# Performance work log

Measured on AMD Instinct MI355X. Metric: run time of the kernel, lower is better.

The kernel has to match this reference:

```python
import jax, jax.numpy as jnp
import numpy as np

N_NODES = 65536
N_EDGES = 786432
N_RELS = 8
IN_DIM = 128
HID = 128
N_CLASSES = 10
N_GRAPHS = 64


def setup_inputs() -> dict:
    key = jax.random.key(0)
    ks = jax.random.split(key, 10)
    h = jax.random.normal(ks[0], (N_NODES, IN_DIM), dtype=jnp.float32)
    s = 1.0 / np.sqrt(IN_DIM)
    W1 = jax.random.normal(ks[1], (N_RELS, IN_DIM, HID), dtype=jnp.float32) * s
    W1_self = jax.random.normal(ks[2], (IN_DIM, HID), dtype=jnp.float32) * s
    b1 = jnp.zeros((HID,), dtype=jnp.float32)
    sh = 1.0 / np.sqrt(HID)
    W2 = jax.random.normal(ks[3], (N_RELS, HID, HID), dtype=jnp.float32) * sh
    W2_self = jax.random.normal(ks[4], (HID, HID), dtype=jnp.float32) * sh
    b2 = jnp.zeros((HID,), dtype=jnp.float32)
    Wc = jax.random.normal(ks[5], (HID, N_CLASSES), dtype=jnp.float32) * sh
    bc = jnp.zeros((N_CLASSES,), dtype=jnp.float32)
    src = jax.random.randint(ks[6], (N_EDGES,), 0, N_NODES, dtype=jnp.int32)
    dst = jax.random.randint(ks[7], (N_EDGES,), 0, N_NODES, dtype=jnp.int32)
    etype = jax.random.randint(ks[8], (N_EDGES,), 0, N_RELS, dtype=jnp.int32)
    # 64 batched graphs of 1024 nodes each (contiguous node blocks)
    graph_ids = (jnp.arange(N_NODES, dtype=jnp.int32) // (N_NODES // N_GRAPHS)).astype(jnp.int32)
    return dict(h=h, W1=W1, W1_self=W1_self, b1=b1, W2=W2, W2_self=W2_self,
                b2=b2, Wc=Wc, bc=bc, src=src, dst=dst, etype=etype,
                graph_ids=graph_ids)


def _relgraphconv(h, W, W_self, b, src, dst, etype):
    # DGL RelGraphConv (regularizer=None, self_loop=True, bias=True, no norm):
    # out[v] = sum_{e: dst(e)=v} W[etype(e)] @ h[src(e)]  +  W_self @ h[v] + b
    # Transform all nodes under each relation (R is small), then gather per-edge.
    xw = jnp.einsum('ni,rio->rno', h, W)          # [R, N, HID]
    msg = xw[etype, src]                           # [E, HID] gather
    agg = jax.ops.segment_sum(msg, dst, num_segments=N_NODES)  # scatter-add
    return agg + h @ W_self + b


def reference(h, W1, W1_self, b1, W2, W2_self, b2, Wc, bc,
              src, dst, etype, graph_ids):
    h1 = jax.nn.relu(_relgraphconv(h, W1, W1_self, b1, src, dst, etype))
    h2 = jax.nn.relu(_relgraphconv(h1, W2, W2_self, b2, src, dst, etype))
    pooled = jax.ops.segment_max(h2, graph_ids, num_segments=N_GRAPHS)  # [G, HID]
    return pooled @ Wc + bc
```

## Files before the change

kernel.cpp:

```cpp
#include <hip/hip_runtime.h>
#include <hip/hip_bf16.h>


#define N_NODES 65536
#define N_EDGES 786432
#define DIM 128
#define NT 9
#define XW_LD (NT * DIM)
#define N_GRAPHS 64

typedef unsigned int uint;
typedef unsigned short ushort;
typedef __attribute__((ext_vector_type(8))) short short8;
typedef __attribute__((ext_vector_type(4))) float f32x4;

__device__ inline ushort f2b(float f) {
  uint u = __float_as_uint(f);
  u += 0x7fff + ((u >> 16) & 1);
  return (ushort)(u >> 16);
}
__device__ inline float b2f(ushort h) { return __uint_as_float(((uint)h) << 16); }
__device__ inline float blo(uint v) { return __uint_as_float(v << 16); }
__device__ inline float bhi(uint v) { return __uint_as_float(v & 0xffff0000u); }

__device__ inline void gl_lds16(const void* g, void* l) {
  __builtin_amdgcn_global_load_lds(
      (const __attribute__((address_space(1))) unsigned int*)g,
      (__attribute__((address_space(3))) unsigned int*)l, 16, 0, 0);
}

__global__ __launch_bounds__(256) void f32_to_bf16_vec(const float* __restrict__ x,
                                                       ushort* __restrict__ y, int n4) {
  int i = blockIdx.x * 256 + threadIdx.x;
  if (i >= n4) return;
  float4 v = ((const float4*)x)[i];
  ushort4 o;
  o.x = f2b(v.x); o.y = f2b(v.y); o.z = f2b(v.z); o.w = f2b(v.w);
  ((ushort4*)y)[i] = o;
}

__global__ __launch_bounds__(256) void wconv_all(const float* __restrict__ W1,
                                                 const float* __restrict__ W1s,
                                                 const float* __restrict__ W2,
                                                 const float* __restrict__ W2s,
                                                 ushort* __restrict__ Wt1,
                                                 ushort* __restrict__ Wt2) {
  int b = blockIdx.x;
  const float* S;
  ushort* D;
  int tile;
  if (b < 9) { D = Wt1; tile = b; S = (b < 8) ? (W1 + (size_t)b * 16384) : W1s; }
  else       { D = Wt2; tile = b - 9; S = (tile < 8) ? (W2 + (size_t)tile * 16384) : W2s; }
  for (int i = threadIdx.x; i < 16384; i += 256) {
    int n = i >> 7, k = i & 127;
    D[((size_t)tile * 128 + n) * 128 + k] = f2b(S[k * 128 + n]);
  }
}

__global__ __launch_bounds__(256) void fill_bins_sliced(const int* __restrict__ src,
                                                        const int* __restrict__ dst,
                                                        const int* __restrict__ et,
                                                        int* __restrict__ cnt,
                                                        uint* __restrict__ bins) {
  int slice = blockIdx.x & 7;
  int e = (blockIdx.x >> 3) * 256 + threadIdx.x;
  if (e >= N_EDGES) return;
  int d = dst[e];
  if ((d >> 13) != slice) return;
  int r = atomicAdd(&cnt[d], 1);
  if (r < 64) bins[((size_t)d << 6) + r] = (uint)src[e] * 576u + (uint)et[e] * 64u;
}

__global__ __launch_bounds__(256, 4) void gemm_bk64(const ushort* __restrict__ A,
                                                    const ushort* __restrict__ Bt,
                                                    ushort* __restrict__ C, int ldc) {
  __shared__ char lds[32768];
  const int bid = blockIdx.x;
  const int swz = (bid & 7) * 576 + (bid >> 3);
  const int bm = swz / 9, bn = swz % 9;
  const char* Ag = (const char*)(A + (size_t)bm * 128 * 128);
  const char* Bg = (const char*)(Bt + (size_t)bn * 128 * 128);
  const int tid = threadIdx.x, wv = tid >> 6, ln = tid & 63;
  const int wm = wv >> 1, wn = wv & 1, lr = ln & 15, kq = ln >> 4;

  f32x4 acc[4][4];
#pragma unroll
  for (int m = 0; m < 4; ++m)
#pragma unroll
    for (int n = 0; n < 4; ++n) acc[m][n] = (f32x4){0.f, 0.f, 0.f, 0.f};

#pragma unroll
  for (int kt = 0; kt < 2; ++kt) {
    if (kt) __syncthreads();
#pragma unroll
    for (int it = 0; it < 4; ++it) {
      int chunk = it * 4096 + wv * 1024;
      int p = chunk + ln * 16;
      int row = p >> 7, inb = p & 127;
      int sw = inb ^ ((row & 7) << 4);
      size_t gb = (size_t)row * 256 + (size_t)kt * 128 + sw;
      gl_lds16(Ag + gb, lds + chunk);
      gl_lds16(Bg + gb, lds + 16384 + chunk);
    }
    asm volatile("s_waitcnt vmcnt(0)" ::: "memory");
    __syncthreads();
#pragma unroll
    for (int k2 = 0; k2 < 2; ++k2) {
      const int kb = k2 * 64 + kq * 16;
      short8 a[4], b[4];
#pragma unroll
      for (int m = 0; m < 4; ++m) {
        int row = wm * 64 + m * 16 + lr;
        a[m] = *(const short8*)(lds + ((row * 128 + kb) ^ ((row & 7) << 4)));
      }
#pragma unroll
      for (int n = 0; n < 4; ++n) {
        int col = wn * 64 + n * 16 + lr;
        b[n] = *(const short8*)(lds + 16384 + ((col * 128 + kb) ^ ((col & 7) << 4)));
      }
#pragma unroll
      for (int m = 0; m < 4; ++m)
#pragma unroll
        for (int n = 0; n < 4; ++n)
          acc[m][n] = __builtin_amdgcn_mfma_f32_16x16x32_bf16(a[m], b[n], acc[m][n], 0, 0, 0);
    }
  }

  __syncthreads();
#pragma unroll
  for (int m = 0; m < 4; ++m) {
    int rb0 = wm * 64 + m * 16 + kq * 4;
#pragma unroll
    for (int n = 0; n < 4; ++n) {
      int col = wn * 64 + n * 16 + lr;
#pragma unroll
      for (int e = 0; e < 4; ++e) {
        int row = rb0 + e;
        int off = (row * 256 + col * 2) ^ ((row & 7) << 4);
        *(ushort*)(lds + off) = f2b(acc[m][n][e]);
      }
    }
  }
  __syncthreads();
  char* Cg = (char*)C + (size_t)(bm * 128) * (size_t)ldc * 2 + (size_t)bn * 256;
#pragma unroll
  for (int it = 0; it < 8; ++it) {
    int p = it * 4096 + tid * 16;
    int row = p >> 8, inb = p & 255;
    short8 v = *(const short8*)(lds + row * 256 + (inb ^ ((row & 7) << 4)));
    *(short8*)(Cg + (size_t)row * (size_t)ldc * 2 + inb) = v;
  }
}

template <bool POOL>
__global__ __launch_bounds__(256) void gather_out(const uint* __restrict__ XWu,
                                                  const uint* __restrict__ bins,
                                                  const int* __restrict__ cnt,
                                                  const float* __restrict__ bias,
                                                  uint* __restrict__ hout,
                                                  ushort* __restrict__ partial2) {
  __shared__ ushort pm[4][128];
  int node = (blockIdx.x * 256 + threadIdx.x) >> 6;
  int w = threadIdx.x >> 6;
  int ln = threadIdx.x & 63;
  int ne = __builtin_amdgcn_readfirstlane(cnt[node]);
  if (ne > 64) ne = 64;
  uint sv = XWu[(size_t)node * 576 + 512 + ln];
  float2 bv = ((const float2*)bias)[ln];
  uint mv = bins[((size_t)node << 6) + ln];
  float2 acc = {0.f, 0.f};

  int i = 0;
  for (; i + 8 <= ne; i += 8) {
    uint v0 = XWu[(uint)__builtin_amdgcn_readlane((int)mv, i + 0) + ln];
    uint v1 = XWu[(uint)__builtin_amdgcn_readlane((int)mv, i + 1) + ln];
    uint v2 = XWu[(uint)__builtin_amdgcn_readlane((int)mv, i + 2) + ln];
    uint v3 = XWu[(uint)__builtin_amdgcn_readlane((int)mv, i + 3) + ln];
    uint v4 = XWu[(uint)__builtin_amdgcn_readlane((int)mv, i + 4) + ln];
    uint v5 = XWu[(uint)__builtin_amdgcn_readlane((int)mv, i + 5) + ln];
    uint v6 = XWu[(uint)__builtin_amdgcn_readlane((int)mv, i + 6) + ln];
    uint v7 = XWu[(uint)__builtin_amdgcn_readlane((int)mv, i + 7) + ln];
    acc.x += blo(v0); acc.y += bhi(v0);
    acc.x += blo(v1); acc.y += bhi(v1);
    acc.x += blo(v2); acc.y += bhi(v2);
    acc.x += blo(v3); acc.y += bhi(v3);
    acc.x += blo(v4); acc.y += bhi(v4);
    acc.x += blo(v5); acc.y += bhi(v5);
    acc.x += blo(v6); acc.y += bhi(v6);
    acc.x += blo(v7); acc.y += bhi(v7);
  }
  for (; i + 4 <= ne; i += 4) {
    uint v0 = XWu[(uint)__builtin_amdgcn_readlane((int)mv, i + 0) + ln];
    uint v1 = XWu[(uint)__builtin_amdgcn_readlane((int)mv, i + 1) + ln];
    uint v2 = XWu[(uint)__builtin_amdgcn_readlane((int)mv, i + 2) + ln];
    uint v3 = XWu[(uint)__builtin_amdgcn_readlane((int)mv, i + 3) + ln];
    acc.x += blo(v0); acc.y += bhi(v0);
    acc.x += blo(v1); acc.y += bhi(v1);
    acc.x += blo(v2); acc.y += bhi(v2);
    acc.x += blo(v3); acc.y += bhi(v3);
  }
  for (; i < ne; ++i) {
    uint v = XWu[(uint)__builtin_amdgcn_readlane((int)mv, i) + ln];
    acc.x += blo(v); acc.y += bhi(v);
  }

  float r0 = fmaxf(acc.x + blo(sv) + bv.x, 0.f);
  float r1 = fmaxf(acc.y + bhi(sv) + bv.y, 0.f);
  if (POOL) {
    pm[w][ln * 2] = f2b(r0);
    pm[w][ln * 2 + 1] = f2b(r1);
    __syncthreads();
    int t = threadIdx.x;
    if (t < 128) {
      float m = fmaxf(fmaxf(b2f(pm[0][t]), b2f(pm[1][t])),
                      fmaxf(b2f(pm[2][t]), b2f(pm[3][t])));
      partial2[(size_t)blockIdx.x * 128 + t] = f2b(m);
    }
  } else {
    hout[(size_t)node * 64 + ln] = (uint)f2b(r0) | ((uint)f2b(r1) << 16);
  }
}

__global__ __launch_bounds__(256) void classify2(const ushort* __restrict__ partial2,
                                                 const float* __restrict__ Wc,
                                                 const float* __restrict__ bc,
                                                 float* __restrict__ out) {
  __shared__ float red[2][128];
  __shared__ float pooled[128];
  int g = blockIdx.x, t = threadIdx.x;
  int d = t & 127, half = t >> 7;
  const ushort* base = partial2 + ((size_t)g * 256 + half * 128) * 128;
  float m = 0.f;
  for (int i = 0; i < 128; ++i) m = fmaxf(m, b2f(base[i * 128 + d]));
  red[half][d] = m;
  __syncthreads();
  if (t < 128) pooled[t] = fmaxf(red[0][t], red[1][t]);
  __syncthreads();
  if (t < 10) {
    float s = bc[t];
    for (int dd = 0; dd < DIM; ++dd) s += pooled[dd] * Wc[dd * 10 + t];
    out[g * 10 + t] = s;
  }
}

extern "C" void kernel_launch(void* const* d_in, const int* in_sizes, int n_in,
                              void* d_out, int out_size, void* d_ws, size_t ws_size,
                              hipStream_t stream) {
  const float* h       = (const float*)d_in[0];
  const float* W1      = (const float*)d_in[1];
  const float* W1_self = (const float*)d_in[2];
  const float* b1      = (const float*)d_in[3];
  const float* W2      = (const float*)d_in[4];
  const float* W2_self = (const float*)d_in[5];
  const float* b2      = (const float*)d_in[6];
  const float* Wc      = (const float*)d_in[7];
  const float* bc      = (const float*)d_in[8];
  const int* src   = (const int*)d_in[9];
  const int* dst   = (const int*)d_in[10];
  const int* etype = (const int*)d_in[11];
  float* out = (float*)d_out;

  char* ws = (char*)d_ws;
  ushort* XW      = (ushort*)(ws);
  ushort* hb      = (ushort*)(ws + 150994944);
  ushort* h1b     = (ushort*)(ws + 167772160);
  ushort* Wt1c    = (ushort*)(ws + 184549376);
  ushort* Wt2c    = (ushort*)(ws + 184844288);
  int*    cnt     = (int*)(ws + 185139200);
  uint*   bins    = (uint*)(ws + 185401344);
  ushort* partial2= (ushort*)(ws + 202178560);

  const int n4_h = N_NODES * DIM / 4;
  const int g_h = n4_h / 256;
  const int g_edge = (N_EDGES + 255) / 256;
  const int g_sliced = g_edge * 8;
  const int g_gather = N_NODES / 4;
  const int g_gemm = (N_NODES / 128) * NT;

  f32_to_bf16_vec<<<g_h, 256, 0, stream>>>(h, hb, n4_h);
  wconv_all<<<18, 256, 0, stream>>>(W1, W1_self, W2, W2_self, Wt1c, Wt2c);

  hipMemsetAsync(cnt, 0, N_NODES * sizeof(int), stream);
  fill_bins_sliced<<<g_sliced, 256, 0, stream>>>(src, dst, etype, cnt, bins);

  gemm_bk64<<<g_gemm, 256, 0, stream>>>(hb, Wt1c, XW, XW_LD);
  gather_out<false><<<g_gather, 256, 0, stream>>>((const uint*)XW, bins, cnt, b1,
                                                  (uint*)h1b, partial2);

  gemm_bk64<<<g_gemm, 256, 0, stream>>>(h1b, Wt2c, XW, XW_LD);
  gather_out<true><<<g_gather, 256, 0, stream>>>((const uint*)XW, bins, cnt, b2,
                                                 (uint*)h1b, partial2);

  classify2<<<N_GRAPHS, 256, 0, stream>>>(partial2, Wc, bc, out);

  (void)in_sizes; (void)n_in; (void)out_size; (void)ws_size;
}
```

Before: 224.8 us.

## Fuse edge binning into first GEMM launch and vectorize dst loads

Merges the sliced edge-binning kernel into the layer-1 GEMM launch as extra trailing blocks, so binning runs alongside the GEMM in one launch instead of serially. Each fill block now handles 1024 edges with int4 loads of dst, four edges per thread, which cuts the fill grid size. Fill blocks reserve the same 32KB of LDS and the same launch bounds as GEMM blocks even though they do not use it, which may limit how many can co-reside. The memset is moved earlier in the stream.

```diff
diff --git a/kernel.cpp b/kernel.cpp
--- a/kernel.cpp
+++ b/kernel.cpp
@@ -8,6 +8,8 @@
 #define NT 9
 #define XW_LD (NT * DIM)
 #define N_GRAPHS 64
+#define G_GEMM 4608
+#define G_FILL 6144
 
 typedef unsigned int uint;
 typedef unsigned short ushort;
@@ -57,25 +59,10 @@
   }
 }
 
-__global__ __launch_bounds__(256) void fill_bins_sliced(const int* __restrict__ src,
-                                                        const int* __restrict__ dst,
-                                                        const int* __restrict__ et,
-                                                        int* __restrict__ cnt,
-                                                        uint* __restrict__ bins) {
-  int slice = blockIdx.x & 7;
-  int e = (blockIdx.x >> 3) * 256 + threadIdx.x;
-  if (e >= N_EDGES) return;
-  int d = dst[e];
-  if ((d >> 13) != slice) return;
-  int r = atomicAdd(&cnt[d], 1);
-  if (r < 64) bins[((size_t)d << 6) + r] = (uint)src[e] * 576u + (uint)et[e] * 64u;
-}
-
-__global__ __launch_bounds__(256, 4) void gemm_bk64(const ushort* __restrict__ A,
-                                                    const ushort* __restrict__ Bt,
-                                                    ushort* __restrict__ C, int ldc) {
-  __shared__ char lds[32768];
-  const int bid = blockIdx.x;
+__device__ __forceinline__ void gemm_body(const ushort* __restrict__ A,
+                                          const ushort* __restrict__ Bt,
+                                          ushort* __restrict__ C, int ldc,
+                                          int bid, char* lds) {
   const int swz = (bid & 7) * 576 + (bid >> 3);
   const int bm = swz / 9, bn = swz % 9;
   const char* Ag = (const char*)(A + (size_t)bm * 128 * 128);
@@ -149,6 +136,48 @@
     int row = p >> 8, inb = p & 255;
     short8 v = *(const short8*)(lds + row * 256 + (inb ^ ((row & 7) << 4)));
     *(short8*)(Cg + (size_t)row * (size_t)ldc * 2 + inb) = v;
+  }
+}
+
+__global__ __launch_bounds__(256, 4) void gemm_bk64(const ushort* __restrict__ A,
+                                                    const ushort* __restrict__ Bt,
+                                                    ushort* __restrict__ C, int ldc) {
+  __shared__ char lds[32768];
+  gemm_body(A, Bt, C, ldc, blockIdx.x, lds);
+}
+
+__global__ __launch_bounds__(256, 4) void gemm1_fill(const ushort* __restrict__ A,
+                                                     const ushort* __restrict__ Bt,
+                                                     ushort* __restrict__ C, int ldc,
+                                                     const int* __restrict__ src,
+                                                     const int* __restrict__ dst,
+                                                     const int* __restrict__ et,
+                                                     int* __restrict__ cnt,
+                                                     uint* __restrict__ bins) {
+  __shared__ char lds[32768];
+  if (blockIdx.x < G_GEMM) {
+    gemm_body(A, Bt, C, ldc, blockIdx.x, lds);
+    return;
+  }
+  const int fb = blockIdx.x - G_GEMM;
+  const int slice = fb & 7;
+  const int e0 = (fb >> 3) * 1024 + threadIdx.x * 4;
+  int4 d4 = *(const int4*)(dst + e0);
+  if ((d4.x >> 13) == slice) {
+    int r = atomicAdd(&cnt[d4.x], 1);
+    if (r < 64) bins[((size_t)d4.x << 6) + r] = (uint)src[e0] * 576u + (uint)et[e0] * 64u;
+  }
+  if ((d4.y >> 13) == slice) {
+    int r = atomicAdd(&cnt[d4.y], 1);
+    if (r < 64) bins[((size_t)d4.y << 6) + r] = (uint)src[e0 + 1] * 576u + (uint)et[e0 + 1] * 64u;
+  }
+  if ((d4.z >> 13) == slice) {
+    int r = atomicAdd(&cnt[d4.z], 1);
+    if (r < 64) bins[((size_t)d4.z << 6) + r] = (uint)src[e0 + 2] * 576u + (uint)et[e0 + 2] * 64u;
+  }
+  if ((d4.w >> 13) == slice) {
+    int r = atomicAdd(&cnt[d4.w], 1);
+    if (r < 64) bins[((size_t)d4.w << 6) + r] = (uint)src[e0 + 3] * 576u + (uint)et[e0 + 3] * 64u;
   }
 }
 
@@ -272,22 +301,18 @@
 
   const int n4_h = N_NODES * DIM / 4;
   const int g_h = n4_h / 256;
-  const int g_edge = (N_EDGES + 255) / 256;
-  const int g_sliced = g_edge * 8;
   const int g_gather = N_NODES / 4;
-  const int g_gemm = (N_NODES / 128) * NT;
-
+
+  hipMemsetAsync(cnt, 0, N_NODES * sizeof(int), stream);
   f32_to_bf16_vec<<<g_h, 256, 0, stream>>>(h, hb, n4_h);
   wconv_all<<<18, 256, 0, stream>>>(W1, W1_self, W2, W2_self, Wt1c, Wt2c);
 
-  hipMemsetAsync(cnt, 0, N_NODES * sizeof(int), stream);
-  fill_bins_sliced<<<g_sliced, 256, 0, stream>>>(src, dst, etype, cnt, bins);
-
-  gemm_bk64<<<g_gemm, 256, 0, stream>>>(hb, Wt1c, XW, XW_LD);
+  gemm1_fill<<<G_GEMM + G_FILL, 256, 0, stream>>>(hb, Wt1c, XW, XW_LD,
+                                                  src, dst, etype, cnt, bins);
   gather_out<false><<<g_gather, 256, 0, stream>>>((const uint*)XW, bins, cnt, b1,
                                                   (uint*)h1b, partial2);
 
-  gemm_bk64<<<g_gemm, 256, 0, stream>>>(h1b, Wt2c, XW, XW_LD);
+  gemm_bk64<<<G_GEMM, 256, 0, stream>>>(h1b, Wt2c, XW, XW_LD);
   gather_out<true><<<g_gather, 256, 0, stream>>>((const uint*)XW, bins, cnt, b2,
                                                  (uint*)h1b, partial2);
 
```

Result: no change. 223.5 us (-0.6%).

## Fuse per-relation aggregation and transform into one RGCN layer kernel

Applied to the files above, without the earlier changes.

Each layer now aggregates neighbour features per relation first and then multiplies by that relation's weight, all inside one fused kernel. This replaces the old scheme of materialising a large bf16 XW tensor holding every node under every relation and then gathering from it. Bins store (src<<3|etype) and are sorted per node by relation in LDS with ballots. The gather for the next relation is double-buffered against the MFMA of the current one, and the self-loop rows are loaded straight into LDS. The change removes the large XW write and re-read, at the cost of serial, latency-bound per-edge gather loops and higher LDS use per block, which may reduce occupancy.

```diff
diff --git a/kernel.cpp b/kernel.cpp
--- a/kernel.cpp
+++ b/kernel.cpp
@@ -5,12 +5,11 @@
 #define N_NODES 65536
 #define N_EDGES 786432
 #define DIM 128
-#define NT 9
-#define XW_LD (NT * DIM)
 #define N_GRAPHS 64
 
 typedef unsigned int uint;
 typedef unsigned short ushort;
+typedef unsigned char uchar;
 typedef __attribute__((ext_vector_type(8))) short short8;
 typedef __attribute__((ext_vector_type(4))) float f32x4;
 
@@ -68,177 +67,171 @@
   int d = dst[e];
   if ((d >> 13) != slice) return;
   int r = atomicAdd(&cnt[d], 1);
-  if (r < 64) bins[((size_t)d << 6) + r] = (uint)src[e] * 576u + (uint)et[e] * 64u;
-}
-
-__global__ __launch_bounds__(256, 4) void gemm_bk64(const ushort* __restrict__ A,
-                                                    const ushort* __restrict__ Bt,
-                                                    ushort* __restrict__ C, int ldc) {
-  __shared__ char lds[32768];
-  const int bid = blockIdx.x;
-  const int swz = (bid & 7) * 576 + (bid >> 3);
-  const int bm = swz / 9, bn = swz % 9;
-  const char* Ag = (const char*)(A + (size_t)bm * 128 * 128);
-  const char* Bg = (const char*)(Bt + (size_t)bn * 128 * 128);
+  if (r < 64) bins[((size_t)d << 6) + r] = ((uint)src[e] << 3) | (uint)et[e];
+}
+
+__device__ __forceinline__ void gather_rel(int wv, int ln, int r,
+                                           const uint* __restrict__ hw,
+                                           const uint* sbin,
+                                           const uchar (*soff)[16],
+                                           char* ab) {
+  for (int k = 0; k < 16; ++k) {
+    int nl = wv * 16 + k;
+    int s = __builtin_amdgcn_readfirstlane((int)soff[nl][r]);
+    int e = __builtin_amdgcn_readfirstlane((int)soff[nl][r + 1]);
+    float ax = 0.f, ay = 0.f;
+    for (int j = s; j < e; ++j) {
+      uint rec = sbin[nl * 64 + j];
+      uint v = hw[(size_t)(rec >> 3) * 64 + ln];
+      ax += blo(v); ay += bhi(v);
+    }
+    uint o = (uint)f2b(ax) | ((uint)f2b(ay) << 16);
+    *(uint*)(ab + nl * 256 + ((ln * 4) ^ ((nl & 15) << 4))) = o;
+  }
+}
+
+template <bool POOL>
+__global__ __launch_bounds__(256) void rgcn_layer(const ushort* __restrict__ hin,
+                                                  const uint* __restrict__ bins,
+                                                  const int* __restrict__ cnt,
+                                                  const ushort* __restrict__ Wt,
+                                                  const float* __restrict__ bias,
+                                                  ushort* __restrict__ hout,
+                                                  float* __restrict__ partial) {
+  __shared__ uint sbin[64 * 64];
+  __shared__ uchar soff[64][16];
+  __shared__ char agg[2][16384];
+
+  const int blk = blockIdx.x, nb = blk * 64;
   const int tid = threadIdx.x, wv = tid >> 6, ln = tid & 63;
-  const int wm = wv >> 1, wn = wv & 1, lr = ln & 15, kq = ln >> 4;
-
-  f32x4 acc[4][4];
+  const int lr = ln & 15, kq = ln >> 4;
+  const uint* hw = (const uint*)hin;
+  unsigned long long lt = (1ull << ln) - 1ull;
+
+  for (int k = 0; k < 16; ++k) {
+    int nl = wv * 16 + k;
+    int node = nb + nl;
+    int ne = cnt[node];
+    if (ne > 64) ne = 64;
+    uint rec = bins[((size_t)node << 6) + ln];
+    bool valid = ln < ne;
+    int key = (int)(rec & 7u);
+    unsigned long long mymask = 0ull;
+    int myoff = 0, run = 0;
+#pragma unroll
+    for (int r = 0; r < 8; ++r) {
+      unsigned long long mr = __ballot(valid && key == r);
+      if (key == r) { mymask = mr; myoff = run; }
+      if (ln == r) soff[nl][r] = (uchar)run;
+      run += __popcll(mr);
+    }
+    if (ln == 8) soff[nl][8] = (uchar)run;
+    if (valid) sbin[nl * 64 + myoff + __popcll(mymask & lt)] = rec;
+  }
+  __syncthreads();
+
+  f32x4 acc[4][2];
 #pragma unroll
   for (int m = 0; m < 4; ++m)
 #pragma unroll
-    for (int n = 0; n < 4; ++n) acc[m][n] = (f32x4){0.f, 0.f, 0.f, 0.f};
-
-#pragma unroll
-  for (int kt = 0; kt < 2; ++kt) {
-    if (kt) __syncthreads();
-#pragma unroll
-    for (int it = 0; it < 4; ++it) {
-      int chunk = it * 4096 + wv * 1024;
-      int p = chunk + ln * 16;
-      int row = p >> 7, inb = p & 127;
-      int sw = inb ^ ((row & 7) << 4);
-      size_t gb = (size_t)row * 256 + (size_t)kt * 128 + sw;
-      gl_lds16(Ag + gb, lds + chunk);
-      gl_lds16(Bg + gb, lds + 16384 + chunk);
+    for (int n = 0; n < 2; ++n) acc[m][n] = (f32x4){0.f, 0.f, 0.f, 0.f};
+
+  gather_rel(wv, ln, 0, hw, sbin, soff, agg[0]);
+  __syncthreads();
+
+  for (int r = 0; r < 9; ++r) {
+    char* cur = agg[r & 1];
+    char* nxt = agg[(r & 1) ^ 1];
+    short8 b[2][4];
+#pragma unroll
+    for (int n = 0; n < 2; ++n) {
+      const ushort* wrow = Wt + ((size_t)(r * 128 + wv * 32 + n * 16 + lr)) * 128;
+#pragma unroll
+      for (int k2 = 0; k2 < 4; ++k2)
+        b[n][k2] = *(const short8*)(wrow + k2 * 32 + kq * 8);
+    }
+    if (r < 7) {
+      gather_rel(wv, ln, r + 1, hw, sbin, soff, nxt);
+    } else if (r == 7) {
+      const char* hbase = (const char*)(hin + (size_t)nb * 128);
+#pragma unroll
+      for (int it = 0; it < 4; ++it) {
+        int p = it * 4096 + tid * 16;
+        int row = p >> 8, inb = p & 255;
+        gl_lds16(hbase + row * 256 + (inb ^ ((row & 15) << 4)), nxt + p);
+      }
+    }
+#pragma unroll
+    for (int k2 = 0; k2 < 4; ++k2) {
+      const int kb = k2 * 64 + kq * 16;
+      short8 a[4];
+#pragma unroll
+      for (int m = 0; m < 4; ++m) {
+        int row = m * 16 + lr;
+        a[m] = *(const short8*)(cur + row * 256 + (kb ^ ((row & 15) << 4)));
+      }
+#pragma unroll
+      for (int m = 0; m < 4; ++m)
+#pragma unroll
+        for (int n = 0; n < 2; ++n)
+          acc[m][n] = __builtin_amdgcn_mfma_f32_16x16x32_bf16(a[m], b[n][k2], acc[m][n], 0, 0, 0);
     }
     asm volatile("s_waitcnt vmcnt(0)" ::: "memory");
     __syncthreads();
-#pragma unroll
-    for (int k2 = 0; k2 < 2; ++k2) {
-      const int kb = k2 * 64 + kq * 16;
-      short8 a[4], b[4];
-#pragma unroll
-      for (int m = 0; m < 4; ++m) {
-        int row = wm * 64 + m * 16 + lr;
-        a[m] = *(const short8*)(lds + ((row * 128 + kb) ^ ((row & 7) << 4)));
+  }
+
+  char* ob = agg[0];
+  float bvals[2];
+#pragma unroll
+  for (int n = 0; n < 2; ++n) bvals[n] = bias[wv * 32 + n * 16 + lr];
+#pragma unroll
+  for (int m = 0; m < 4; ++m) {
+#pragma unroll
+    for (int n = 0; n < 2; ++n) {
+      int colb = (wv * 32 + n * 16 + lr) * 2;
+#pragma unroll
+      for (int e = 0; e < 4; ++e) {
+        int row = m * 16 + kq * 4 + e;
+        float v = fmaxf(acc[m][n][e] + bvals[n], 0.f);
+        *(ushort*)(ob + ((row * 256 + colb) ^ ((row & 15) << 4))) = f2b(v);
       }
-#pragma unroll
-      for (int n = 0; n < 4; ++n) {
-        int col = wn * 64 + n * 16 + lr;
-        b[n] = *(const short8*)(lds + 16384 + ((col * 128 + kb) ^ ((col & 7) << 4)));
-      }
-#pragma unroll
-      for (int m = 0; m < 4; ++m)
-#pragma unroll
-        for (int n = 0; n < 4; ++n)
-          acc[m][n] = __builtin_amdgcn_mfma_f32_16x16x32_bf16(a[m], b[n], acc[m][n], 0, 0, 0);
-    }
-  }
-
-  __syncthreads();
-#pragma unroll
-  for (int m = 0; m < 4; ++m) {
-    int rb0 = wm * 64 + m * 16 + kq * 4;
-#pragma unroll
-    for (int n = 0; n < 4; ++n) {
-      int col = wn * 64 + n * 16 + lr;
-#pragma unroll
-      for (int e = 0; e < 4; ++e) {
-        int row = rb0 + e;
-        int off = (row * 256 + col * 2) ^ ((row & 7) << 4);
-        *(ushort*)(lds + off) = f2b(acc[m][n][e]);
-      }
-    }
-  }
-  __syncthreads();
-  char* Cg = (char*)C + (size_t)(bm * 128) * (size_t)ldc * 2 + (size_t)bn * 256;
-#pragma unroll
-  for (int it = 0; it < 8; ++it) {
-    int p = it * 4096 + tid * 16;
-    int row = p >> 8, inb = p & 255;
-    short8 v = *(const short8*)(lds + row * 256 + (inb ^ ((row & 7) << 4)));
-    *(short8*)(Cg + (size_t)row * (size_t)ldc * 2 + inb) = v;
-  }
-}
-
-template <bool POOL>
-__global__ __launch_bounds__(256) void gather_out(const uint* __restrict__ XWu,
-                                                  const uint* __restrict__ bins,
-                                                  const int* __restrict__ cnt,
-                                                  const float* __restrict__ bias,
-                                                  uint* __restrict__ hout,
-                                                  ushort* __restrict__ partial2) {
-  __shared__ ushort pm[4][128];
-  int node = (blockIdx.x * 256 + threadIdx.x) >> 6;
-  int w = threadIdx.x >> 6;
-  int ln = threadIdx.x & 63;
-  int ne = __builtin_amdgcn_readfirstlane(cnt[node]);
-  if (ne > 64) ne = 64;
-  uint sv = XWu[(size_t)node * 576 + 512 + ln];
-  float2 bv = ((const float2*)bias)[ln];
-  uint mv = bins[((size_t)node << 6) + ln];
-  float2 acc = {0.f, 0.f};
-
-  int i = 0;
-  for (; i + 8 <= ne; i += 8) {
-    uint v0 = XWu[(uint)__builtin_amdgcn_readlane((int)mv, i + 0) + ln];
-    uint v1 = XWu[(uint)__builtin_amdgcn_readlane((int)mv, i + 1) + ln];
-    uint v2 = XWu[(uint)__builtin_amdgcn_readlane((int)mv, i + 2) + ln];
-    uint v3 = XWu[(uint)__builtin_amdgcn_readlane((int)mv, i + 3) + ln];
-    uint v4 = XWu[(uint)__builtin_amdgcn_readlane((int)mv, i + 4) + ln];
-    uint v5 = XWu[(uint)__builtin_amdgcn_readlane((int)mv, i + 5) + ln];
-    uint v6 = XWu[(uint)__builtin_amdgcn_readlane((int)mv, i + 6) + ln];
-    uint v7 = XWu[(uint)__builtin_amdgcn_readlane((int)mv, i + 7) + ln];
-    acc.x += blo(v0); acc.y += bhi(v0);
-    acc.x += blo(v1); acc.y += bhi(v1);
-    acc.x += blo(v2); acc.y += bhi(v2);
-    acc.x += blo(v3); acc.y += bhi(v3);
-    acc.x += blo(v4); acc.y += bhi(v4);
-    acc.x += blo(v5); acc.y += bhi(v5);
-    acc.x += blo(v6); acc.y += bhi(v6);
-    acc.x += blo(v7); acc.y += bhi(v7);
-  }
-  for (; i + 4 <= ne; i += 4) {
-    uint v0 = XWu[(uint)__builtin_amdgcn_readlane((int)mv, i + 0) + ln];
-    uint v1 = XWu[(uint)__builtin_amdgcn_readlane((int)mv, i + 1) + ln];
-    uint v2 = XWu[(uint)__builtin_amdgcn_readlane((int)mv, i + 2) + ln];
-    uint v3 = XWu[(uint)__builtin_amdgcn_readlane((int)mv, i + 3) + ln];
-    acc.x += blo(v0); acc.y += bhi(v0);
-    acc.x += blo(v1); acc.y += bhi(v1);
-    acc.x += blo(v2); acc.y += bhi(v2);
-    acc.x += blo(v3); acc.y += bhi(v3);
-  }
-  for (; i < ne; ++i) {
-    uint v = XWu[(uint)__builtin_amdgcn_readlane((int)mv, i) + ln];
-    acc.x += blo(v); acc.y += bhi(v);
-  }
-
-  float r0 = fmaxf(acc.x + blo(sv) + bv.x, 0.f);
-  float r1 = fmaxf(acc.y + bhi(sv) + bv.y, 0.f);
-  if (POOL) {
-    pm[w][ln * 2] = f2b(r0);
-    pm[w][ln * 2 + 1] = f2b(r1);
-    __syncthreads();
-    int t = threadIdx.x;
-    if (t < 128) {
-      float m = fmaxf(fmaxf(b2f(pm[0][t]), b2f(pm[1][t])),
-                      fmaxf(b2f(pm[2][t]), b2f(pm[3][t])));
-      partial2[(size_t)blockIdx.x * 128 + t] = f2b(m);
+    }
+  }
+  __syncthreads();
+  if (!POOL) {
+    char* dst = (char*)hout + (size_t)nb * 256;
+#pragma unroll
+    for (int it = 0; it < 4; ++it) {
+      int p = it * 4096 + tid * 16;
+      int row = p >> 8, inb = p & 255;
+      short8 v = *(const short8*)(ob + row * 256 + (inb ^ ((row & 15) << 4)));
+      *(short8*)(dst + (size_t)row * 256 + inb) = v;
     }
   } else {
-    hout[(size_t)node * 64 + ln] = (uint)f2b(r0) | ((uint)f2b(r1) << 16);
-  }
-}
-
-__global__ __launch_bounds__(256) void classify2(const ushort* __restrict__ partial2,
-                                                 const float* __restrict__ Wc,
-                                                 const float* __restrict__ bc,
-                                                 float* __restrict__ out) {
-  __shared__ float red[2][128];
+    if (tid < 128) {
+      float m = 0.f;
+      for (int row = 0; row < 64; ++row)
+        m = fmaxf(m, b2f(*(const ushort*)(ob + ((row * 256 + tid * 2) ^ ((row & 15) << 4)))));
+      partial[(size_t)blk * 128 + tid] = m;
+    }
+  }
+}
+
+__global__ __launch_bounds__(128) void classify(const float* __restrict__ partial,
+                                                const float* __restrict__ Wc,
+                                                const float* __restrict__ bc,
+                                                float* __restrict__ out) {
   __shared__ float pooled[128];
   int g = blockIdx.x, t = threadIdx.x;
-  int d = t & 127, half = t >> 7;
-  const ushort* base = partial2 + ((size_t)g * 256 + half * 128) * 128;
+  const float* p = partial + (size_t)g * 16 * 128;
   float m = 0.f;
-  for (int i = 0; i < 128; ++i) m = fmaxf(m, b2f(base[i * 128 + d]));
-  red[half][d] = m;
-  __syncthreads();
-  if (t < 128) pooled[t] = fmaxf(red[0][t], red[1][t]);
+#pragma unroll
+  for (int i = 0; i < 16; ++i) m = fmaxf(m, p[i * 128 + t]);
+  pooled[t] = m;
   __syncthreads();
   if (t < 10) {
     float s = bc[t];
-    for (int dd = 0; dd < DIM; ++dd) s += pooled[dd] * Wc[dd * 10 + t];
+    for (int d = 0; d < DIM; ++d) s += pooled[d] * Wc[d * 10 + t];
     out[g * 10 + t] = s;
   }
 }
@@ -261,37 +254,29 @@
   float* out = (float*)d_out;
 
   char* ws = (char*)d_ws;
-  ushort* XW      = (ushort*)(ws);
-  ushort* hb      = (ushort*)(ws + 150994944);
-  ushort* h1b     = (ushort*)(ws + 167772160);
-  ushort* Wt1c    = (ushort*)(ws + 184549376);
-  ushort* Wt2c    = (ushort*)(ws + 184844288);
-  int*    cnt     = (int*)(ws + 185139200);
-  uint*   bins    = (uint*)(ws + 185401344);
-  ushort* partial2= (ushort*)(ws + 202178560);
+  ushort* hb      = (ushort*)(ws);
+  ushort* h1b     = (ushort*)(ws + 16777216);
+  ushort* Wt1c    = (ushort*)(ws + 33554432);
+  ushort* Wt2c    = (ushort*)(ws + 33849344);
+  int*    cnt     = (int*)(ws + 34144256);
+  uint*   bins    = (uint*)(ws + 34406400);
+  float*  partial = (float*)(ws + 51183616);
 
   const int n4_h = N_NODES * DIM / 4;
   const int g_h = n4_h / 256;
   const int g_edge = (N_EDGES + 255) / 256;
   const int g_sliced = g_edge * 8;
-  const int g_gather = N_NODES / 4;
-  const int g_gemm = (N_NODES / 128) * NT;
-
+  const int g_layer = N_NODES / 64;
+
+  hipMemsetAsync(cnt, 0, N_NODES * sizeof(int), stream);
   f32_to_bf16_vec<<<g_h, 256, 0, stream>>>(h, hb, n4_h);
   wconv_all<<<18, 256, 0, stream>>>(W1, W1_self, W2, W2_self, Wt1c, Wt2c);
-
-  hipMemsetAsync(cnt, 0, N_NODES * sizeof(int), stream);
   fill_bins_sliced<<<g_sliced, 256, 0, stream>>>(src, dst, etype, cnt, bins);
 
-  gemm_bk64<<<g_gemm, 256, 0, stream>>>(hb, Wt1c, XW, XW_LD);
-  gather_out<false><<<g_gather, 256, 0, stream>>>((const uint*)XW, bins, cnt, b1,
-                                                  (uint*)h1b, partial2);
-
-  gemm_bk64<<<g_gemm, 256, 0, stream>>>(h1b, Wt2c, XW, XW_LD);
-  gather_out<true><<<g_gather, 256, 0, stream>>>((const uint*)XW, bins, cnt, b2,
-                                                 (uint*)h1b, partial2);
-
-  classify2<<<N_GRAPHS, 256, 0, stream>>>(partial2, Wc, bc, out);
+  rgcn_layer<false><<<g_layer, 256, 0, stream>>>(hb, bins, cnt, Wt1c, b1, h1b, partial);
+  rgcn_layer<true><<<g_layer, 256, 0, stream>>>(h1b, bins, cnt, Wt2c, b2, h1b, partial);
+
+  classify<<<N_GRAPHS, 128, 0, stream>>>(partial, Wc, bc, out);
 
   (void)in_sizes; (void)n_in; (void)out_size; (void)ws_size;
 }
```

After: 509.6 us. +126.7%, slower.
